# Kernel tuning notes

Hardware: AMD Instinct MI355X
Metric: run time of the kernel (lower is better)

Reference implementation:

```python
import jax, jax.numpy as jnp
import numpy as np

T, N, E, IN_DIM, OUT_DIM, K = 4, 50000, 800000, 128, 128, 3


def setup_inputs() -> dict:
    key = jax.random.key(0)
    ks = jax.random.split(key, 6)
    x = jax.random.normal(ks[0], (T, N, IN_DIM), dtype=jnp.float32)
    edge_row = jax.random.randint(ks[1], (E,), 0, N, dtype=jnp.int64)
    edge_col = jax.random.randint(ks[2], (E,), 0, N, dtype=jnp.int64)
    edge_val = jax.random.uniform(ks[3], (E,), dtype=jnp.float32)
    # xavier_uniform per [in,out] slice: bound = sqrt(6/(in+out))
    bound = float(np.sqrt(6.0 / (IN_DIM + OUT_DIM)))
    weight = jax.random.uniform(ks[4], (T, K, IN_DIM, OUT_DIM), dtype=jnp.float32,
                                minval=-bound, maxval=bound)
    bias = jnp.zeros((T, OUT_DIM), dtype=jnp.float32)
    return {"x": x, "edge_row": edge_row, "edge_col": edge_col,
            "edge_val": edge_val, "weight": weight, "bias": bias}


def _spmm_batched(edge_row, edge_col, edge_val, h):
    # h: [T, N, C]; sparse A (COO) applied to flattened [N, T*C] features
    t, n, c = h.shape
    h_flat = jnp.transpose(h, (1, 0, 2)).reshape(n, t * c)      # [N, T*C]
    msg = edge_val[:, None] * h_flat[edge_col]                  # [E, T*C]
    out = jax.ops.segment_sum(msg, edge_row, num_segments=n)    # [N, T*C]
    return jnp.transpose(out.reshape(n, t, c), (1, 0, 2))       # [T, N, C]


def reference(x, edge_row, edge_col, edge_val, weight, bias):
    # Chebyshev recurrence: T_0 = x, T_1 = L x, T_k = 2 L T_{k-1} - T_{k-2}
    tx_0 = x
    out = jnp.einsum('tni,tio->tno', tx_0, weight[:, 0])
    tx_1 = _spmm_batched(edge_row, edge_col, edge_val, x)
    out = out + jnp.einsum('tni,tio->tno', tx_1, weight[:, 1])
    for k in range(2, K):
        tx_2 = 2.0 * _spmm_batched(edge_row, edge_col, edge_val, tx_1) - tx_0
        out = out + jnp.einsum('tni,tio->tno', tx_2, weight[:, k])
        tx_0, tx_1 = tx_1, tx_2
    return out + bias[:, None, :]
```

## Files before the change

### kernel.cpp

```cpp
#include <hip/hip_runtime.h>
#include <hip/hip_bf16.h>

#define T_ 4
#define N_ 50000
#define E_ 800000
#define C_ 128
#define K_ 3
#define UNROLL_ 8

typedef __hip_bfloat16 bf16;
typedef __attribute__((ext_vector_type(4))) float f32x4;
typedef __attribute__((ext_vector_type(8))) short bf16x8;
typedef __attribute__((ext_vector_type(4))) short s16x4;

__device__ inline short bf16bits(float f) {
    bf16 h = __float2bfloat16(f);
    union { bf16 h; short s; } u; u.h = h; return u.s;
}
__device__ inline float bf16f(short s) {
    union { bf16 h; short s; } u; u.s = s; return __bfloat162float(u.h);
}


__global__ void count_kernel(const int* __restrict__ row, int* __restrict__ counts) {
    int e = blockIdx.x * blockDim.x + threadIdx.x;
    if (e < E_) atomicAdd(&counts[row[e]], 1);
}

__global__ __launch_bounds__(1024) void scan_kernel(const int* __restrict__ counts,
                                                    int* __restrict__ starts,
                                                    int* __restrict__ cursors) {
    __shared__ int wsum[16];
    __shared__ int carry_s;
    int tid = threadIdx.x;
    int wave = tid >> 6, lane = tid & 63;
    if (tid == 0) carry_s = 0;
    __syncthreads();
    for (int base = 0; base < N_; base += 1024) {
        int i = base + tid;
        int v = (i < N_) ? counts[i] : 0;
        int s = v;
        #pragma unroll
        for (int off = 1; off < 64; off <<= 1) {
            int u = __shfl_up(s, off, 64);
            if (lane >= off) s += u;
        }
        if (lane == 63) wsum[wave] = s;
        __syncthreads();
        if (wave == 0) {
            int w = (lane < 16) ? wsum[lane] : 0;
            #pragma unroll
            for (int off = 1; off < 16; off <<= 1) {
                int u = __shfl_up(w, off, 64);
                if (lane >= off) w += u;
            }
            if (lane < 16) wsum[lane] = w;
        }
        __syncthreads();
        int carry = carry_s;
        int wbase = (wave == 0) ? 0 : wsum[wave - 1];
        int incl = carry + wbase + s;
        if (i < N_) {
            starts[i]  = incl - v;
            cursors[i] = incl - v;
        }
        __syncthreads();
        if (tid == 1023) carry_s = incl;
        __syncthreads();
    }
    if (tid == 0) starts[N_] = carry_s;
}

__global__ void scatter_kernel(const int* __restrict__ row, const int* __restrict__ col,
                               const float* __restrict__ val, int* __restrict__ cursors,
                               int* __restrict__ scol, float* __restrict__ sval) {
    int e = blockIdx.x * blockDim.x + threadIdx.x;
    if (e < E_) {
        int p = atomicAdd(&cursors[row[e]], 1);
        scol[p] = col[e];
        sval[p] = val[e];
    }
}


__global__ __launch_bounds__(128) void spmm1_kernel(const int* __restrict__ starts,
                                                    const int* __restrict__ scol,
                                                    const float* __restrict__ sval,
                                                    const float* __restrict__ x,
                                                    bf16* __restrict__ tx1) {
    int n   = blockIdx.x;
    int tid = threadIdx.x;
    int t = tid >> 5, c = (tid & 31) * 4;
    int s  = starts[n];
    int e1 = starts[n + 1];
    const float* xt = x + (size_t)t * (N_ * C_) + c;
    f32x4 acc = {0.f, 0.f, 0.f, 0.f};
    for (int e = s; e < e1; e += UNROLL_) {
        int   cc[UNROLL_];
        float vv[UNROLL_];
        #pragma unroll
        for (int j = 0; j < UNROLL_; ++j) {
            int ee = e + j;
            bool ok = ee < e1;
            cc[j] = ok ? scol[ee] : 0;
            vv[j] = ok ? sval[ee] : 0.f;
        }
        f32x4 g[UNROLL_];
        #pragma unroll
        for (int j = 0; j < UNROLL_; ++j)
            g[j] = *(const f32x4*)(xt + (size_t)cc[j] * C_);
        #pragma unroll
        for (int j = 0; j < UNROLL_; ++j)
            acc += g[j] * vv[j];
    }
    s16x4 o;
    #pragma unroll
    for (int j = 0; j < 4; ++j) o[j] = bf16bits(acc[j]);
    *(s16x4*)(tx1 + (size_t)t * (N_ * C_) + (size_t)n * C_ + c) = o;
}


__global__ __launch_bounds__(128) void spmm2_kernel(const int* __restrict__ starts,
                                                    const int* __restrict__ scol,
                                                    const float* __restrict__ sval,
                                                    const bf16* __restrict__ tx1,
                                                    const float* __restrict__ x,
                                                    bf16* __restrict__ tx2) {
    int n   = blockIdx.x;
    int tid = threadIdx.x;
    int t = tid >> 5, c = (tid & 31) * 4;
    int s  = starts[n];
    int e1 = starts[n + 1];
    const bf16* ht = tx1 + (size_t)t * (N_ * C_) + c;
    f32x4 acc = {0.f, 0.f, 0.f, 0.f};
    for (int e = s; e < e1; e += UNROLL_) {
        int   cc[UNROLL_];
        float vv[UNROLL_];
        #pragma unroll
        for (int j = 0; j < UNROLL_; ++j) {
            int ee = e + j;
            bool ok = ee < e1;
            cc[j] = ok ? scol[ee] : 0;
            vv[j] = ok ? sval[ee] : 0.f;
        }
        s16x4 g[UNROLL_];
        #pragma unroll
        for (int j = 0; j < UNROLL_; ++j)
            g[j] = *(const s16x4*)(ht + (size_t)cc[j] * C_);
        #pragma unroll
        for (int j = 0; j < UNROLL_; ++j) {
            #pragma unroll
            for (int q = 0; q < 4; ++q)
                acc[q] += vv[j] * bf16f(g[j][q]);
        }
    }
    size_t oi = (size_t)t * (N_ * C_) + (size_t)n * C_ + c;
    f32x4 xv = *(const f32x4*)(x + oi);
    s16x4 o;
    #pragma unroll
    for (int j = 0; j < 4; ++j) o[j] = bf16bits(2.f * acc[j] - xv[j]);
    *(s16x4*)(tx2 + oi) = o;
}


__global__ __launch_bounds__(256) void gemm_kernel(const float* __restrict__ x,
                                                   const bf16* __restrict__ tx1,
                                                   const bf16* __restrict__ tx2,
                                                   const float* __restrict__ weight,
                                                   const float* __restrict__ bias,
                                                   float* __restrict__ out) {
    int t  = blockIdx.y;
    int m0 = blockIdx.x * 128;
    __shared__ short As[128][40];
    __shared__ short Bs[128][40];
    int tid  = threadIdx.x;
    int wave = tid >> 6, lane = tid & 63;
    int l15 = lane & 15, l4 = lane >> 4;

    f32x4 acc[2][8];
    for (int i = 0; i < 2; ++i)
        for (int j = 0; j < 8; ++j) acc[i][j] = (f32x4){0.f, 0.f, 0.f, 0.f};

    size_t tslice = (size_t)t * N_ * C_;

    for (int ks = 0; ks < 12; ++ks) {
        int sid = ks >> 2;
        int i0  = (ks & 3) * 32;
        for (int slot = tid; slot < 512; slot += 256) {
            int r = slot >> 2, seg = slot & 3;
            int gr = m0 + r;
            int4 v = {0, 0, 0, 0};
            if (gr < N_) {
                if (sid == 0) {
                    const float* p = x + tslice + (size_t)gr * C_ + i0 + seg * 8;
                    union { int4 v; short s[8]; } u;
                    #pragma unroll
                    for (int j = 0; j < 8; ++j) u.s[j] = bf16bits(p[j]);
                    v = u.v;
                } else {
                    const bf16* p = (sid == 1 ? tx1 : tx2) + tslice + (size_t)gr * C_ + i0 + seg * 8;
                    v = *(const int4*)p;
                }
            }
            *(int4*)&As[r][seg * 8] = v;
        }
        const float* W = weight + (((size_t)t * K_ + sid) * C_ + i0) * C_;
        for (int slot = tid; slot < 512; slot += 256) {
            int r = slot >> 4, seg = slot & 15;
            const float* p = W + (size_t)r * C_ + seg * 8;
            #pragma unroll
            for (int j = 0; j < 8; ++j) Bs[seg * 8 + j][r] = bf16bits(p[j]);
        }
        __syncthreads();

        int krow = l4 * 8;
        bf16x8 bfr[8];
        #pragma unroll
        for (int nf = 0; nf < 8; ++nf)
            bfr[nf] = *(bf16x8*)&Bs[nf * 16 + l15][krow];
        #pragma unroll
        for (int mf = 0; mf < 2; ++mf) {
            bf16x8 a = *(bf16x8*)&As[wave * 32 + mf * 16 + l15][krow];
            #pragma unroll
            for (int nf = 0; nf < 8; ++nf)
                acc[mf][nf] = __builtin_amdgcn_mfma_f32_16x16x32_bf16(a, bfr[nf], acc[mf][nf], 0, 0, 0);
        }
        __syncthreads();
    }

    const float* bs = bias + (size_t)t * C_;
    float* ot = out + tslice;
    #pragma unroll
    for (int nf = 0; nf < 8; ++nf) {
        int gc = nf * 16 + l15;
        float bv = bs[gc];
        #pragma unroll
        for (int mf = 0; mf < 2; ++mf) {
            #pragma unroll
            for (int reg = 0; reg < 4; ++reg) {
                int gr = m0 + wave * 32 + mf * 16 + l4 * 4 + reg;
                if (gr < N_) ot[(size_t)gr * C_ + gc] = acc[mf][nf][reg] + bv;
            }
        }
    }
}


extern "C" void kernel_launch(void* const* d_in, const int* in_sizes, int n_in,
                              void* d_out, int out_size, void* d_ws, size_t ws_size,
                              hipStream_t stream) {
    const float* x      = (const float*)d_in[0];
    const int*   erow   = (const int*)d_in[1];
    const int*   ecol   = (const int*)d_in[2];
    const float* eval   = (const float*)d_in[3];
    const float* weight = (const float*)d_in[4];
    const float* bias   = (const float*)d_in[5];
    float* out = (float*)d_out;

    char* ws = (char*)d_ws;
    size_t off = 0;
    auto alloc = [&](size_t bytes) -> void* {
        void* p = ws + off;
        off += (bytes + 255) & ~(size_t)255;
        return p;
    };
    int*   counts  = (int*)alloc((N_ + 1) * sizeof(int));
    int*   starts  = (int*)alloc((N_ + 1) * sizeof(int));
    int*   cursors = (int*)alloc((size_t)N_ * sizeof(int));
    int*   scol    = (int*)alloc((size_t)E_ * sizeof(int));
    float* sval    = (float*)alloc((size_t)E_ * sizeof(float));
    bf16*  tx1     = (bf16*)alloc((size_t)T_ * N_ * C_ * sizeof(bf16));
    bf16*  tx2     = (bf16*)alloc((size_t)T_ * N_ * C_ * sizeof(bf16));

    hipMemsetAsync(counts, 0, (N_ + 1) * sizeof(int), stream);
    count_kernel<<<(E_ + 255) / 256, 256, 0, stream>>>(erow, counts);
    scan_kernel<<<1, 1024, 0, stream>>>(counts, starts, cursors);
    scatter_kernel<<<(E_ + 255) / 256, 256, 0, stream>>>(erow, ecol, eval, cursors, scol, sval);
    spmm1_kernel<<<N_, 128, 0, stream>>>(starts, scol, sval, x, tx1);
    spmm2_kernel<<<N_, 128, 0, stream>>>(starts, scol, sval, tx1, x, tx2);
    dim3 g((N_ + 127) / 128, T_);
    gemm_kernel<<<g, 256, 0, stream>>>(x, tx1, tx2, weight, bias, out);
}
```

Baseline: 781.8 us.

## Interleave features as [N,T*C] bf16 and fold Chebyshev combination into weights

Converts x to a bf16 node-major [N, T*C] buffer so each SpMM gathers one contiguous 1 KB row per edge instead of four strided fp32 slices. A single generic spmm kernel now computes L·x and L·L·x, and the -x and 2× terms of the recurrence move into the GEMM weights (W0-W2, W1, 2W2). This removes the fp32 gathers and the extra x read in the second SpMM, at the cost of an extra conversion pass and bf16 rounding of the first-hop input.

```diff
diff --git a/kernel.cpp b/kernel.cpp
--- a/kernel.cpp
+++ b/kernel.cpp
@@ -6,6 +6,7 @@
 #define E_ 800000
 #define C_ 128
 #define K_ 3
+#define TC_ 512
 #define UNROLL_ 8
 
 typedef __hip_bfloat16 bf16;
@@ -83,17 +84,29 @@
 }
 
 
-__global__ __launch_bounds__(128) void spmm1_kernel(const int* __restrict__ starts,
-                                                    const int* __restrict__ scol,
-                                                    const float* __restrict__ sval,
-                                                    const float* __restrict__ x,
-                                                    bf16* __restrict__ tx1) {
+__global__ __launch_bounds__(256) void convert_kernel(const float* __restrict__ x,
+                                                      bf16* __restrict__ xb) {
+    int t   = blockIdx.y;
+    int idx = blockIdx.x * 256 + threadIdx.x;
+    int n = idx >> 5, q = idx & 31;
+    f32x4 v = *(const f32x4*)(x + ((size_t)t * N_ + n) * C_ + q * 4);
+    s16x4 o;
+    #pragma unroll
+    for (int j = 0; j < 4; ++j) o[j] = bf16bits(v[j]);
+    *(s16x4*)(xb + (size_t)n * TC_ + t * C_ + q * 4) = o;
+}
+
+
+__global__ __launch_bounds__(128) void spmm_kernel(const int* __restrict__ starts,
+                                                   const int* __restrict__ scol,
+                                                   const float* __restrict__ sval,
+                                                   const bf16* __restrict__ src,
+                                                   bf16* __restrict__ dst) {
     int n   = blockIdx.x;
-    int tid = threadIdx.x;
-    int t = tid >> 5, c = (tid & 31) * 4;
+    int ch  = threadIdx.x * 4;
     int s  = starts[n];
     int e1 = starts[n + 1];
-    const float* xt = x + (size_t)t * (N_ * C_) + c;
+    const bf16* sb = src + ch;
     f32x4 acc = {0.f, 0.f, 0.f, 0.f};
     for (int e = s; e < e1; e += UNROLL_) {
         int   cc[UNROLL_];
@@ -105,67 +118,27 @@
             cc[j] = ok ? scol[ee] : 0;
             vv[j] = ok ? sval[ee] : 0.f;
         }
-        f32x4 g[UNROLL_];
+        s16x4 g[UNROLL_];
         #pragma unroll
         for (int j = 0; j < UNROLL_; ++j)
-            g[j] = *(const f32x4*)(xt + (size_t)cc[j] * C_);
-        #pragma unroll
-        for (int j = 0; j < UNROLL_; ++j)
-            acc += g[j] * vv[j];
+            g[j] = *(const s16x4*)(sb + (size_t)cc[j] * TC_);
+        #pragma unroll
+        for (int j = 0; j < UNROLL_; ++j) {
+            #pragma unroll
+            for (int q = 0; q < 4; ++q)
+                acc[q] += vv[j] * bf16f(g[j][q]);
+        }
     }
     s16x4 o;
     #pragma unroll
     for (int j = 0; j < 4; ++j) o[j] = bf16bits(acc[j]);
-    *(s16x4*)(tx1 + (size_t)t * (N_ * C_) + (size_t)n * C_ + c) = o;
-}
-
-
-__global__ __launch_bounds__(128) void spmm2_kernel(const int* __restrict__ starts,
-                                                    const int* __restrict__ scol,
-                                                    const float* __restrict__ sval,
-                                                    const bf16* __restrict__ tx1,
-                                                    const float* __restrict__ x,
-                                                    bf16* __restrict__ tx2) {
-    int n   = blockIdx.x;
-    int tid = threadIdx.x;
-    int t = tid >> 5, c = (tid & 31) * 4;
-    int s  = starts[n];
-    int e1 = starts[n + 1];
-    const bf16* ht = tx1 + (size_t)t * (N_ * C_) + c;
-    f32x4 acc = {0.f, 0.f, 0.f, 0.f};
-    for (int e = s; e < e1; e += UNROLL_) {
-        int   cc[UNROLL_];
-        float vv[UNROLL_];
-        #pragma unroll
-        for (int j = 0; j < UNROLL_; ++j) {
-            int ee = e + j;
-            bool ok = ee < e1;
-            cc[j] = ok ? scol[ee] : 0;
-            vv[j] = ok ? sval[ee] : 0.f;
-        }
-        s16x4 g[UNROLL_];
-        #pragma unroll
-        for (int j = 0; j < UNROLL_; ++j)
-            g[j] = *(const s16x4*)(ht + (size_t)cc[j] * C_);
-        #pragma unroll
-        for (int j = 0; j < UNROLL_; ++j) {
-            #pragma unroll
-            for (int q = 0; q < 4; ++q)
-                acc[q] += vv[j] * bf16f(g[j][q]);
-        }
-    }
-    size_t oi = (size_t)t * (N_ * C_) + (size_t)n * C_ + c;
-    f32x4 xv = *(const f32x4*)(x + oi);
-    s16x4 o;
-    #pragma unroll
-    for (int j = 0; j < 4; ++j) o[j] = bf16bits(2.f * acc[j] - xv[j]);
-    *(s16x4*)(tx2 + oi) = o;
+    *(s16x4*)(dst + (size_t)n * TC_ + ch) = o;
 }
 
 
 __global__ __launch_bounds__(256) void gemm_kernel(const float* __restrict__ x,
-                                                   const bf16* __restrict__ tx1,
-                                                   const bf16* __restrict__ tx2,
+                                                   const bf16* __restrict__ tx1b,
+                                                   const bf16* __restrict__ ub,
                                                    const float* __restrict__ weight,
                                                    const float* __restrict__ bias,
                                                    float* __restrict__ out) {
@@ -198,7 +171,7 @@
                     for (int j = 0; j < 8; ++j) u.s[j] = bf16bits(p[j]);
                     v = u.v;
                 } else {
-                    const bf16* p = (sid == 1 ? tx1 : tx2) + tslice + (size_t)gr * C_ + i0 + seg * 8;
+                    const bf16* p = (sid == 1 ? tx1b : ub) + (size_t)gr * TC_ + t * C_ + i0 + seg * 8;
                     v = *(const int4*)p;
                 }
             }
@@ -209,7 +182,13 @@
             int r = slot >> 4, seg = slot & 15;
             const float* p = W + (size_t)r * C_ + seg * 8;
             #pragma unroll
-            for (int j = 0; j < 8; ++j) Bs[seg * 8 + j][r] = bf16bits(p[j]);
+            for (int j = 0; j < 8; ++j) {
+                float w;
+                if (sid == 0)      w = p[j] - p[j + 2 * C_ * C_];
+                else if (sid == 1) w = p[j];
+                else               w = 2.f * p[j];
+                Bs[seg * 8 + j][r] = bf16bits(w);
+            }
         }
         __syncthreads();
 
@@ -269,15 +248,17 @@
     int*   cursors = (int*)alloc((size_t)N_ * sizeof(int));
     int*   scol    = (int*)alloc((size_t)E_ * sizeof(int));
     float* sval    = (float*)alloc((size_t)E_ * sizeof(float));
-    bf16*  tx1     = (bf16*)alloc((size_t)T_ * N_ * C_ * sizeof(bf16));
-    bf16*  tx2     = (bf16*)alloc((size_t)T_ * N_ * C_ * sizeof(bf16));
+    bf16*  bufA    = (bf16*)alloc((size_t)N_ * TC_ * sizeof(bf16));
+    bf16*  bufB    = (bf16*)alloc((size_t)N_ * TC_ * sizeof(bf16));
 
     hipMemsetAsync(counts, 0, (N_ + 1) * sizeof(int), stream);
     count_kernel<<<(E_ + 255) / 256, 256, 0, stream>>>(erow, counts);
     scan_kernel<<<1, 1024, 0, stream>>>(counts, starts, cursors);
     scatter_kernel<<<(E_ + 255) / 256, 256, 0, stream>>>(erow, ecol, eval, cursors, scol, sval);
-    spmm1_kernel<<<N_, 128, 0, stream>>>(starts, scol, sval, x, tx1);
-    spmm2_kernel<<<N_, 128, 0, stream>>>(starts, scol, sval, tx1, x, tx2);
+    dim3 cg(N_ * 32 / 256, T_);
+    convert_kernel<<<cg, 256, 0, stream>>>(x, bufA);
+    spmm_kernel<<<N_, 128, 0, stream>>>(starts, scol, sval, bufA, bufB);
+    spmm_kernel<<<N_, 128, 0, stream>>>(starts, scol, sval, bufB, bufA);
     dim3 g((N_ + 127) / 128, T_);
-    gemm_kernel<<<g, 256, 0, stream>>>(x, tx1, tx2, weight, bias, out);
-}
+    gemm_kernel<<<g, 256, 0, stream>>>(x, bufB, bufA, weight, bias, out);
+}
```

New measurement: 812.5 us. +3.9%, slower.
